# Optimization experiments

Hardware: AMD Instinct MI355X
Metric: run time of the kernel (lower is better)

The kernel has to match this reference:

```python
import jax, jax.numpy as jnp
import numpy as np

HEADS = 12
HEAD_DIM = 64  # dim=768 // heads=12
NEG = -1e9


def setup_inputs() -> dict:
    key = jax.random.key(0)
    k1, k2, k3 = jax.random.split(key, 3)
    dim = HEADS * HEAD_DIM
    x = jax.random.normal(k1, (8, 1024, dim), dtype=jnp.float32)
    W_qkv = jax.random.normal(k2, (dim, 3 * dim), dtype=jnp.float32) * (dim ** -0.5)
    b_qkv = jnp.zeros((3 * dim,), dtype=jnp.float32)
    W_out = jax.random.normal(k3, (dim, dim), dtype=jnp.float32) * (dim ** -0.5)
    b_out = jnp.zeros((dim,), dtype=jnp.float32)
    return {"x": x, "W_qkv": W_qkv, "b_qkv": b_qkv, "W_out": W_out, "b_out": b_out}


def reference(x, W_qkv, b_qkv, W_out, b_out):
    B, T, C = x.shape
    qkv = x @ W_qkv + b_qkv                      # [B,T,3C]
    q, k, v = jnp.split(qkv, 3, axis=-1)
    # [B,T,C] -> [B,H,T,Dh]
    def split_heads(t):
        return t.reshape(B, T, HEADS, HEAD_DIM).transpose(0, 2, 1, 3)
    q, k, v = split_heads(q), split_heads(k), split_heads(v)
    att = jnp.einsum('bhqd,bhkd->bhqk', q, k) / jnp.sqrt(jnp.float32(HEAD_DIM))
    causal = jnp.tril(jnp.ones((T, T), dtype=bool))  # [T,T]
    att = jnp.where(causal[None, None], att, NEG)
    att = jax.nn.softmax(att, axis=-1)
    out = jnp.einsum('bhqk,bhkd->bhqd', att, v)  # [B,H,T,Dh]
    out = out.transpose(0, 2, 1, 3).reshape(B, T, C)
    return out @ W_out + b_out
```

## Files before the change

### kernel.cpp

```cpp
#include <hip/hip_runtime.h>
#include <hip/hip_bf16.h>

typedef unsigned short u16;
typedef unsigned int u32;
typedef __attribute__((ext_vector_type(8))) short short8;
typedef __attribute__((ext_vector_type(4))) float f32x4;
typedef __attribute__((ext_vector_type(16))) float f32x16;
typedef __attribute__((ext_vector_type(4))) unsigned int uint4v;

__device__ __forceinline__ u16 f2bf(float f) {
    union { float f; unsigned int u; } v; v.f = f;
    unsigned int u = v.u;
    return (u16)((u + 0x7FFFu + ((u >> 16) & 1u)) >> 16);
}
__device__ __forceinline__ u32 pk2(float a, float b) {
    return ((u32)f2bf(b) << 16) | (u32)f2bf(a);
}
__device__ __forceinline__ void gload_lds16(const u16* g, u16* l) {
    __builtin_amdgcn_global_load_lds((const __attribute__((address_space(1))) void*)g,
                                     (__attribute__((address_space(3))) void*)l, 16, 0, 0);
}

__global__ void k_convert(const float* __restrict__ x, u16* __restrict__ o, int n4) {
    int i = blockIdx.x * blockDim.x + threadIdx.x;
    if (i < n4) {
        float4 v = ((const float4*)x)[i];
        ushort4 r;
        r.x = f2bf(v.x); r.y = f2bf(v.y); r.z = f2bf(v.z); r.w = f2bf(v.w);
        ((ushort4*)o)[i] = r;
    }
}

__global__ void k_transpose_bf(const float* __restrict__ W, u16* __restrict__ Wt, int K, int N) {
    __shared__ u16 t[32][33];
    int n0 = blockIdx.x * 32, k0 = blockIdx.y * 32;
    int tx = threadIdx.x, ty = threadIdx.y;
    #pragma unroll
    for (int i = 0; i < 4; i++) {
        t[ty + i * 8][tx] = f2bf(W[(long)(k0 + ty + i * 8) * N + n0 + tx]);
    }
    __syncthreads();
    #pragma unroll
    for (int i = 0; i < 4; i++) {
        Wt[(long)(n0 + ty + i * 8) * K + k0 + tx] = t[tx][ty + i * 8];
    }
}

template<int EPI>
__global__ __launch_bounds__(256) void k_gemm_bt(
    const u16* __restrict__ A, const u16* __restrict__ Bt, const float* __restrict__ bias,
    float* __restrict__ Cf, u16* __restrict__ q_out, u16* __restrict__ k_out, u16* __restrict__ vt_out,
    int M, int N, int K)
{
    __shared__ u16 lA[2][128][32];
    __shared__ u16 lB[2][128][32];
    int tid = threadIdx.x;
    int wid = tid >> 6, lane = tid & 63;
    int wm = wid >> 1, wn = wid & 1;
    int ln = lane & 15, gp = lane >> 4;
    int gm0 = blockIdx.x * 128, gn0 = blockIdx.y * 128;

    f32x4 zf = {0.f, 0.f, 0.f, 0.f};
    f32x4 acc[4][4];
    #pragma unroll
    for (int i = 0; i < 4; i++)
        #pragma unroll
        for (int j = 0; j < 4; j++) acc[i][j] = zf;

    int srow = wid * 32 + (lane >> 2);
    int scol = (((lane & 3) ^ ((lane >> 3) & 3))) * 8;
    const u16* gA0 = &A [(size_t)(gm0 + srow) * K + scol];
    const u16* gA1 = gA0 + (size_t)16 * K;
    const u16* gB0 = &Bt[(size_t)(gn0 + srow) * K + scol];
    const u16* gB1 = gB0 + (size_t)16 * K;

    int rc = (gp ^ ((ln >> 1) & 3)) * 8;

    auto stage = [&](int k0, int bb) {
        gload_lds16(gA0 + k0, &lA[bb][wid * 32][0]);
        gload_lds16(gA1 + k0, &lA[bb][wid * 32 + 16][0]);
        gload_lds16(gB0 + k0, &lB[bb][wid * 32][0]);
        gload_lds16(gB1 + k0, &lB[bb][wid * 32 + 16][0]);
    };
    auto compute = [&](int bb) {
        short8 af[4], bfr[4];
        #pragma unroll
        for (int i = 0; i < 4; i++) {
            af[i]  = *(const short8*)&lA[bb][wm * 64 + i * 16 + ln][rc];
            bfr[i] = *(const short8*)&lB[bb][wn * 64 + i * 16 + ln][rc];
        }
        #pragma unroll
        for (int i = 0; i < 4; i++)
            #pragma unroll
            for (int j = 0; j < 4; j++)
                acc[i][j] = __builtin_amdgcn_mfma_f32_16x16x32_bf16(af[i], bfr[j], acc[i][j], 0, 0, 0);
    };

    int nk = K >> 5;
    stage(0, 0);
    asm volatile("s_waitcnt vmcnt(0)" ::: "memory");
    __syncthreads();
    for (int t = 0; t < nk; t += 2) {
        stage((t + 1) << 5, 1);
        compute(0);
        asm volatile("s_waitcnt vmcnt(0)" ::: "memory");
        __syncthreads();
        if (t + 2 < nk) stage((t + 2) << 5, 0);
        compute(1);
        asm volatile("s_waitcnt vmcnt(0)" ::: "memory");
        __syncthreads();
    }

    #pragma unroll
    for (int i = 0; i < 4; i++) {
        #pragma unroll
        for (int j = 0; j < 4; j++) {
            #pragma unroll
            for (int r = 0; r < 4; r++) {
                int m = gm0 + wm * 64 + i * 16 + gp * 4 + r;
                int n = gn0 + wn * 64 + j * 16 + ln;
                float v = acc[i][j][r] + bias[n];
                if (EPI == 0) {
                    Cf[(long)m * N + n] = v;
                } else {
                    int b = m >> 10, t = m & 1023;
                    int which = n / 768, c = n % 768;
                    int h = c >> 6, d = c & 63;
                    int bh = b * 12 + h;
                    u16 bv = f2bf(v);
                    if (which == 0)      q_out[((long)bh * 1024 + t) * 64 + d] = bv;
                    else if (which == 1) k_out[((long)bh * 1024 + t) * 64 + d] = bv;
                    else                 vt_out[((long)bh * 64 + d) * 1024 + t] = bv;
                }
            }
        }
    }
}

__global__ __launch_bounds__(256) void k_attn(
    const u16* __restrict__ Q, const u16* __restrict__ Kb, const u16* __restrict__ Vt,
    u16* __restrict__ O)
{
    int tid = threadIdx.x, w = tid >> 6, lane = tid & 63;
    int l31 = lane & 31, hi = lane >> 5;
    int bx = blockIdx.x;
    int g = bx / 96, bh = bx - g * 96;
    int qt = g + 8 * w, q0 = qt * 32;
    int b = bh / 12, h = bh - b * 12;
    const u16* Qb  = Q  + (size_t)bh * 65536;
    const u16* Kbb = Kb + (size_t)bh * 65536;
    const u16* Vb  = Vt + (size_t)bh * 65536;

    short8 qf[4];
    #pragma unroll
    for (int ch = 0; ch < 4; ch++)
        qf[ch] = *(const short8*)&Qb[(q0 + l31) * 64 + ch * 16 + hi * 8];

    f32x16 o0 = {}, o1 = {};
    float mrun = -INFINITY, lsum = 0.f;
    const float SC = 0.18033688011f;

    int nit = qt + 1;
    for (int it = 0; it < nit; it++) {
        int kt = it * 32;
        f32x16 s = {};
        #pragma unroll
        for (int ch = 0; ch < 4; ch++) {
            short8 kf = *(const short8*)&Kbb[(kt + l31) * 64 + ch * 16 + hi * 8];
            s = __builtin_amdgcn_mfma_f32_32x32x16_bf16(kf, qf[ch], s, 0, 0, 0);
        }
        float ps[16];
        int qg = q0 + l31;
        #pragma unroll
        for (int r = 0; r < 16; r++) {
            int krow = kt + (r & 3) + 8 * (r >> 2) + 4 * hi;
            ps[r] = (krow <= qg) ? s[r] * SC : -1e30f;
        }
        float t8[8];
        #pragma unroll
        for (int i = 0; i < 8; i++) t8[i] = fmaxf(ps[i], ps[i + 8]);
        float t4a = fmaxf(t8[0], t8[1]), t4b = fmaxf(t8[2], t8[3]);
        float t4c = fmaxf(t8[4], t8[5]), t4d = fmaxf(t8[6], t8[7]);
        float tm = fmaxf(fmaxf(t4a, t4b), fmaxf(t4c, t4d));
        tm = fmaxf(tm, __shfl_xor(tm, 32));
        float mn = fmaxf(mrun, tm);
        float scale = exp2f(mrun - mn);
        mrun = mn;
        float rs = 0.f;
        #pragma unroll
        for (int r = 0; r < 16; r++) { ps[r] = exp2f(ps[r] - mn); rs += ps[r]; }
        rs += __shfl_xor(rs, 32);
        lsum = lsum * scale + rs;
        #pragma unroll
        for (int r = 0; r < 16; r++) { o0[r] *= scale; o1[r] *= scale; }
        u32 c[8], sw[8];
        #pragma unroll
        for (int i = 0; i < 8; i++) c[i] = pk2(ps[2 * i], ps[2 * i + 1]);
        #pragma unroll
        for (int i = 0; i < 8; i++) sw[i] = (u32)__shfl_xor((int)c[i], 32);
        union { u32 u[4]; short8 s8; } pb0, pb1;
        pb0.u[0] = hi ? sw[2] : c[0];
        pb0.u[1] = hi ? sw[3] : c[1];
        pb0.u[2] = hi ? c[2]  : sw[0];
        pb0.u[3] = hi ? c[3]  : sw[1];
        pb1.u[0] = hi ? sw[6] : c[4];
        pb1.u[1] = hi ? sw[7] : c[5];
        pb1.u[2] = hi ? c[6]  : sw[4];
        pb1.u[3] = hi ? c[7]  : sw[5];
        #pragma unroll
        for (int kh = 0; kh < 2; kh++) {
            const short8* pbp = kh ? &pb1.s8 : &pb0.s8;
            short8 vf0 = *(const short8*)&Vb[(size_t)l31 * 1024 + kt + kh * 16 + hi * 8];
            short8 vf1 = *(const short8*)&Vb[(size_t)(32 + l31) * 1024 + kt + kh * 16 + hi * 8];
            o0 = __builtin_amdgcn_mfma_f32_32x32x16_bf16(vf0, *pbp, o0, 0, 0, 0);
            o1 = __builtin_amdgcn_mfma_f32_32x32x16_bf16(vf1, *pbp, o1, 0, 0, 0);
        }
    }

    float inv = 1.0f / lsum;
    int t = q0 + l31;
    size_t base = ((size_t)(b * 1024 + t)) * 768 + h * 64;
    #pragma unroll
    for (int rq = 0; rq < 4; rq++) {
        ushort4 u0, u1;
        u0.x = f2bf(o0[4 * rq + 0] * inv); u0.y = f2bf(o0[4 * rq + 1] * inv);
        u0.z = f2bf(o0[4 * rq + 2] * inv); u0.w = f2bf(o0[4 * rq + 3] * inv);
        u1.x = f2bf(o1[4 * rq + 0] * inv); u1.y = f2bf(o1[4 * rq + 1] * inv);
        u1.z = f2bf(o1[4 * rq + 2] * inv); u1.w = f2bf(o1[4 * rq + 3] * inv);
        *(ushort4*)&O[base + rq * 8 + hi * 4]      = u0;
        *(ushort4*)&O[base + 32 + rq * 8 + hi * 4] = u1;
    }
}

extern "C" void kernel_launch(void* const* d_in, const int* in_sizes, int n_in,
                              void* d_out, int out_size, void* d_ws, size_t ws_size,
                              hipStream_t stream)
{
    const float* x     = (const float*)d_in[0];
    const float* W_qkv = (const float*)d_in[1];
    const float* b_qkv = (const float*)d_in[2];
    const float* W_out = (const float*)d_in[3];
    const float* b_out = (const float*)d_in[4];
    float* out = (float*)d_out;

    char* w = (char*)d_ws;
    u16* xb  = (u16*)w; w += (size_t)8192 * 768 * 2;
    u16* wqt = (u16*)w; w += (size_t)2304 * 768 * 2;
    u16* wot = (u16*)w; w += (size_t)768 * 768 * 2;
    u16* qb  = (u16*)w; w += (size_t)96 * 1024 * 64 * 2;
    u16* kb  = (u16*)w; w += (size_t)96 * 1024 * 64 * 2;
    u16* vt  = (u16*)w; w += (size_t)96 * 64 * 1024 * 2;
    u16* ao  = (u16*)w; w += (size_t)8192 * 768 * 2;

    k_convert<<<dim3(6144), 256, 0, stream>>>(x, xb, 1572864);
    k_transpose_bf<<<dim3(72, 24), dim3(32, 8), 0, stream>>>(W_qkv, wqt, 768, 2304);
    k_transpose_bf<<<dim3(24, 24), dim3(32, 8), 0, stream>>>(W_out, wot, 768, 768);
    k_gemm_bt<1><<<dim3(64, 18), 256, 0, stream>>>(xb, wqt, b_qkv, nullptr, qb, kb, vt, 8192, 2304, 768);
    k_attn<<<dim3(768), 256, 0, stream>>>(qb, kb, vt, ao);
    k_gemm_bt<0><<<dim3(64, 6), 256, 0, stream>>>(ao, wot, b_out, out, nullptr, nullptr, nullptr, 8192, 768, 768);
}
```

Before: 162.9 us.

## Triple-buffer GEMM LDS staging with partial vmcnt waits and MFMA priority

```diff
diff --git a/kernel.cpp b/kernel.cpp
--- a/kernel.cpp
+++ b/kernel.cpp
@@ -7,6 +7,9 @@
 typedef __attribute__((ext_vector_type(4))) float f32x4;
 typedef __attribute__((ext_vector_type(16))) float f32x16;
 typedef __attribute__((ext_vector_type(4))) unsigned int uint4v;
+
+#define VMW(n) asm volatile("s_waitcnt vmcnt(" #n ")" ::: "memory")
+#define BARRIER() do { asm volatile("" ::: "memory"); __builtin_amdgcn_s_barrier(); } while (0)
 
 __device__ __forceinline__ u16 f2bf(float f) {
     union { float f; unsigned int u; } v; v.f = f;
@@ -52,8 +55,8 @@
     float* __restrict__ Cf, u16* __restrict__ q_out, u16* __restrict__ k_out, u16* __restrict__ vt_out,
     int M, int N, int K)
 {
-    __shared__ u16 lA[2][128][32];
-    __shared__ u16 lB[2][128][32];
+    __shared__ u16 lA[3][128][32];
+    __shared__ u16 lB[3][128][32];
     int tid = threadIdx.x;
     int wid = tid >> 6, lane = tid & 63;
     int wm = wid >> 1, wn = wid & 1;
@@ -89,26 +92,35 @@
             af[i]  = *(const short8*)&lA[bb][wm * 64 + i * 16 + ln][rc];
             bfr[i] = *(const short8*)&lB[bb][wn * 64 + i * 16 + ln][rc];
         }
+        __builtin_amdgcn_s_setprio(1);
         #pragma unroll
         for (int i = 0; i < 4; i++)
             #pragma unroll
             for (int j = 0; j < 4; j++)
                 acc[i][j] = __builtin_amdgcn_mfma_f32_16x16x32_bf16(af[i], bfr[j], acc[i][j], 0, 0, 0);
+        __builtin_amdgcn_s_setprio(0);
     };
 
     int nk = K >> 5;
     stage(0, 0);
-    asm volatile("s_waitcnt vmcnt(0)" ::: "memory");
-    __syncthreads();
-    for (int t = 0; t < nk; t += 2) {
-        stage((t + 1) << 5, 1);
-        compute(0);
-        asm volatile("s_waitcnt vmcnt(0)" ::: "memory");
-        __syncthreads();
-        if (t + 2 < nk) stage((t + 2) << 5, 0);
-        compute(1);
-        asm volatile("s_waitcnt vmcnt(0)" ::: "memory");
-        __syncthreads();
+    stage(32, 1);
+    stage(64, 2);
+    VMW(8);
+    BARRIER();
+    #pragma unroll 3
+    for (int t = 0; t < nk; ++t) {
+        int c = t % 3;
+        compute(c);
+        BARRIER();
+        if (t + 3 < nk) {
+            stage((t + 3) << 5, c);
+            VMW(8);
+        } else if (t + 2 < nk) {
+            VMW(4);
+        } else {
+            VMW(0);
+        }
+        BARRIER();
     }
 
     #pragma unroll
```

After: 156.6 us. 3.9% less time.
